# Performance work log

Measured on AMD Instinct MI355X. Metric: run time of the kernel, lower is better.

Reference implementation:

```python
import jax, jax.numpy as jnp
import numpy as np

N = 100000   # nodes
E = 640000   # edges
G = 256      # graphs in batch
H = 128      # hidden_dim
OUT = 128    # output_dim
IN = 1       # input_dim ('standard' encoding)


def _linear_init(k, din, dout):
    # torch nn.Linear default: U(-1/sqrt(din), 1/sqrt(din)) for weight and bias
    s = 1.0 / np.sqrt(din)
    kw, kb = jax.random.split(k)
    W = jax.random.uniform(kw, (din, dout), jnp.float32, -s, s)
    b = jax.random.uniform(kb, (dout,), jnp.float32, -s, s)
    return W, b


def setup_inputs() -> dict:
    key = jax.random.key(0)
    ks = jax.random.split(key, 10)
    x = jax.random.normal(ks[0], (N, IN), jnp.float32)
    edge_index = jax.random.randint(ks[1], (2, E), 0, N, dtype=jnp.int64)
    batch = jnp.sort(jax.random.randint(ks[2], (N,), 0, G, dtype=jnp.int64))
    inp = {"x": x, "edge_index": edge_index, "batch": batch}
    dims_in = [IN, H, H]  # layer 0 takes input_dim, rest take hidden_dim
    i = 3
    for l, din in enumerate(dims_in):
        inp[f"W1_{l}"], inp[f"b1_{l}"] = _linear_init(ks[i], din, H); i += 1
        inp[f"W2_{l}"], inp[f"b2_{l}"] = _linear_init(ks[i], H, H); i += 1
    inp["Wfc"], inp["bfc"] = _linear_init(ks[i], H, OUT)
    return inp


def reference(x, edge_index, batch,
              W1_0, b1_0, W2_0, b2_0,
              W1_1, b1_1, W2_1, b2_1,
              W1_2, b1_2, W2_2, b2_2,
              Wfc, bfc):
    src, dst = edge_index[0], edge_index[1]

    def gin_conv(h, W1, b1, W2, b2):
        # GINConv, eps=0: out = MLP(h + sum_{j->i} h_j)
        agg = jax.ops.segment_sum(h[src], dst, num_segments=N)  # scatter-add messages
        z = h + agg
        return jnp.maximum(z @ W1 + b1, 0.0) @ W2 + b2

    h = gin_conv(x, W1_0, b1_0, W2_0, b2_0)
    h = gin_conv(h, W1_1, b1_1, W2_1, b2_1)
    h = gin_conv(h, W1_2, b1_2, W2_2, b2_2)
    pooled = jax.ops.segment_sum(h, batch, num_segments=G)  # global_add_pool -> [G, H]
    return pooled @ Wfc + bfc  # [G, OUT]
```

## Files before the change

### kernel.cpp

```cpp
#include <hip/hip_runtime.h>

#define HH 128
#define GG 256
#define CAP 32
#define PSPLIT 16

using f32x4  = __attribute__((ext_vector_type(4))) float;
using bf16x4 = __attribute__((ext_vector_type(4))) __bf16;
using bf16x8 = __attribute__((ext_vector_type(8))) __bf16;

static __device__ __forceinline__ float bf2f(unsigned int u) {
    unsigned int x = u << 16;
    return __builtin_bit_cast(float, x);
}
static __device__ __forceinline__ unsigned short f2bf(float f) {
    __bf16 b = (__bf16)f;
    return __builtin_bit_cast(unsigned short, b);
}

__global__ __launch_bounds__(256) void prep_k(
    int* __restrict__ cnt, float* __restrict__ pooled, int n,
    const float* __restrict__ Wa, const float* __restrict__ Wb,
    const float* __restrict__ Wc, const float* __restrict__ Wd,
    const float* __restrict__ We, __bf16* __restrict__ Wp,
    const int* __restrict__ batch, int* __restrict__ bound, int zb)
{
    const int t = threadIdx.x, b = blockIdx.x;
    if (b < zb) {
        const int i = b * 256 + t;
        if (i < n) cnt[i] = 0;
        if (i < GG * HH) pooled[i] = 0.f;
    } else if (b < zb + 40) {
        const int which = b - zb;
        const int mat = which >> 3;
        const float* W = (mat == 0) ? Wa : (mat == 1) ? Wb : (mat == 2) ? Wc
                       : (mat == 3) ? Wd : We;
        const int slot = (which & 7) * 256 + t;
        const int frag = slot >> 6, lane = slot & 63;
        const int mb = frag >> 2, kb = frag & 3;
        const int col = mb * 16 + (lane & 15);
        const int k0  = kb * 32 + (lane >> 4) * 8;
        bf16x8 v;
        #pragma unroll
        for (int j = 0; j < 8; ++j) v[j] = (__bf16)W[(k0 + j) * HH + col];
        *(bf16x8*)&Wp[(size_t)mat * 16384 + slot * 8] = v;
    } else {
        const int g = t;
        int lo = 0, hi = n;
        while (lo < hi) { int m = (lo + hi) >> 1; if (batch[m] < g) lo = m + 1; else hi = m; }
        bound[g] = lo;
        if (g == 0) bound[GG] = n;
    }
}

__global__ __launch_bounds__(256) void fill_k(const int* __restrict__ src,
                                              const int* __restrict__ dst,
                                              int* __restrict__ cnt,
                                              int* __restrict__ slotbuf, int ne)
{
    int e = blockIdx.x * 256 + threadIdx.x;
    if (e < ne) {
        const int d = dst[e];
        const int off = atomicAdd(&cnt[d], 1);
        if (off < CAP) slotbuf[d * CAP + off] = src[e];
    }
}

__global__ __launch_bounds__(256) void l0_k(
    const float* __restrict__ x,
    const int* __restrict__ cnt, const int* __restrict__ slotbuf,
    const float* __restrict__ W1, const float* __restrict__ b1,
    const __bf16* __restrict__ Wp2, const float* __restrict__ b2,
    unsigned short* __restrict__ hout, int n)
{
    __shared__ __bf16 Wl[16384];
    __shared__ unsigned short tt[4][4096];
    __shared__ float b1l[HH], b2l[HH], w1l[HH];

    const int t    = threadIdx.x;
    const int lane = t & 63, wv = t >> 6;
    const int l16  = lane & 15, lq = lane >> 4;
    const int r0    = blockIdx.x * 128 + wv * 32;
    const int nodeA = r0 + l16, nodeB = r0 + 16 + l16;
    const int rowA  = min(nodeA, n - 1), rowB = min(nodeB, n - 1);
    const int swz   = (l16 & 7) << 4;

    #pragma unroll
    for (int i = 0; i < 8; ++i)
        *(int4*)&Wl[(i * 256 + t) * 8] = *(const int4*)&Wp2[(i * 256 + t) * 8];
    if (t < HH) { b2l[t] = b2[t]; b1l[t] = b1[t]; w1l[t] = W1[t]; }

    float sA, sB;
    {
        float s0 = x[rowA], s1 = 0.f, s2 = 0.f, s3 = 0.f;
        const int dA = min(cnt[rowA], CAP);
        const int* sp = &slotbuf[rowA * CAP];
        for (int j = 0; j < dA; j += 4) {
            const int i1 = min(j + 1, dA - 1), i2 = min(j + 2, dA - 1), i3 = min(j + 3, dA - 1);
            const float v0 = x[sp[j]],  v1 = x[sp[i1]];
            const float v2 = x[sp[i2]], v3 = x[sp[i3]];
            s0 += v0;
            s1 += (j + 1 < dA) ? v1 : 0.f;
            s2 += (j + 2 < dA) ? v2 : 0.f;
            s3 += (j + 3 < dA) ? v3 : 0.f;
        }
        sA = (s0 + s1) + (s2 + s3);
        s0 = x[rowB]; s1 = s2 = s3 = 0.f;
        const int dB = min(cnt[rowB], CAP);
        const int* sq = &slotbuf[rowB * CAP];
        for (int j = 0; j < dB; j += 4) {
            const int i1 = min(j + 1, dB - 1), i2 = min(j + 2, dB - 1), i3 = min(j + 3, dB - 1);
            const float v0 = x[sq[j]],  v1 = x[sq[i1]];
            const float v2 = x[sq[i2]], v3 = x[sq[i3]];
            s0 += v0;
            s1 += (j + 1 < dB) ? v1 : 0.f;
            s2 += (j + 2 < dB) ? v2 : 0.f;
            s3 += (j + 3 < dB) ? v3 : 0.f;
        }
        sB = (s0 + s1) + (s2 + s3);
    }
    __syncthreads();

    char* tl = (char*)tt[wv];
    #pragma unroll
    for (int mt = 0; mt < 8; ++mt) {
        const f32x4 w  = *(const f32x4*)&w1l[mt * 16 + lq * 4];
        const f32x4 bb = *(const f32x4*)&b1l[mt * 16 + lq * 4];
        bf16x4 pa, pb;
        #pragma unroll
        for (int r = 0; r < 4; ++r) {
            pa[r] = (__bf16)fmaxf(fmaf(sA, w[r], bb[r]), 0.f);
            pb[r] = (__bf16)fmaxf(fmaf(sB, w[r], bb[r]), 0.f);
        }
        *(bf16x4*)(tl + ((l16 * 256 + mt * 32 + lq * 8) ^ swz)) = pa;
        *(bf16x4*)(tl + (((16 + l16) * 256 + mt * 32 + lq * 8) ^ swz)) = pb;
    }
    __syncthreads();

    bf16x8 tfA[4], tfB[4];
    #pragma unroll
    for (int kb = 0; kb < 4; ++kb) {
        tfA[kb] = *(const bf16x8*)(tl + ((l16 * 256 + kb * 64 + lq * 16) ^ swz));
        tfB[kb] = *(const bf16x8*)(tl + (((16 + l16) * 256 + kb * 64 + lq * 16) ^ swz));
    }
    f32x4 a2A[8], a2B[8];
    #pragma unroll
    for (int mb = 0; mb < 8; ++mb) {
        const f32x4 bb = *(const f32x4*)&b2l[mb * 16 + lq * 4];
        a2A[mb] = bb; a2B[mb] = bb;
    }
    #pragma unroll
    for (int mb = 0; mb < 8; ++mb)
        #pragma unroll
        for (int kb = 0; kb < 4; ++kb) {
            const bf16x8 wf = *(const bf16x8*)&Wl[((mb * 4 + kb) * 64 + lane) * 8];
            a2A[mb] = __builtin_amdgcn_mfma_f32_16x16x32_bf16(wf, tfA[kb], a2A[mb], 0, 0, 0);
            a2B[mb] = __builtin_amdgcn_mfma_f32_16x16x32_bf16(wf, tfB[kb], a2B[mb], 0, 0, 0);
        }
    if (nodeA < n) {
        #pragma unroll
        for (int mb = 0; mb < 8; ++mb) {
            bf16x4 p;
            #pragma unroll
            for (int r = 0; r < 4; ++r) p[r] = (__bf16)a2A[mb][r];
            *(bf16x4*)&hout[(size_t)nodeA * HH + mb * 16 + lq * 4] = p;
        }
    }
    if (nodeB < n) {
        #pragma unroll
        for (int mb = 0; mb < 8; ++mb) {
            bf16x4 p;
            #pragma unroll
            for (int r = 0; r < 4; ++r) p[r] = (__bf16)a2B[mb][r];
            *(bf16x4*)&hout[(size_t)nodeB * HH + mb * 16 + lq * 4] = p;
        }
    }
}

static __device__ __forceinline__ void agg_body(
    const unsigned short* __restrict__ h, const int* __restrict__ cnt,
    const int* __restrict__ slotbuf, unsigned short* __restrict__ z, int n)
{
    const int wave = (blockIdx.x * 256 + threadIdx.x) >> 6;
    const int lane = threadIdx.x & 63;
    const int half = lane >> 5, sl = lane & 31;
    const int nw   = (gridDim.x * 256) >> 6;
    const int npairs = (n + 1) >> 1;
    const uint2* h8 = (const uint2*)h;
    uint2* z8 = (uint2*)z;

    for (int pr = wave; pr < npairs; pr += nw) {
        const int node = min(2 * pr + half, n - 1);
        const int deg = min(cnt[node], CAP);
        const int* sp = &slotbuf[node * CAP];
        const uint2 su = h8[(size_t)node * 32 + sl];
        float a0 = bf2f(su.x & 0xffff), a1 = bf2f(su.x >> 16);
        float a2 = bf2f(su.y & 0xffff), a3 = bf2f(su.y >> 16);
        float b0 = 0.f, b1 = 0.f, b2 = 0.f, b3 = 0.f;
        float c0 = 0.f, c1 = 0.f, c2 = 0.f, c3 = 0.f;
        float d0 = 0.f, d1 = 0.f, d2 = 0.f, d3 = 0.f;
        for (int j = 0; j < deg; j += 4) {
            const int i1 = min(j + 1, deg - 1), i2 = min(j + 2, deg - 1), i3 = min(j + 3, deg - 1);
            const uint2 v0 = h8[(size_t)sp[j]  * 32 + sl];
            const uint2 v1 = h8[(size_t)sp[i1] * 32 + sl];
            const uint2 v2 = h8[(size_t)sp[i2] * 32 + sl];
            const uint2 v3 = h8[(size_t)sp[i3] * 32 + sl];
            a0 += bf2f(v0.x & 0xffff); a1 += bf2f(v0.x >> 16);
            a2 += bf2f(v0.y & 0xffff); a3 += bf2f(v0.y >> 16);
            const bool m1 = (j + 1 < deg), m2 = (j + 2 < deg), m3 = (j + 3 < deg);
            b0 += m1 ? bf2f(v1.x & 0xffff) : 0.f; b1 += m1 ? bf2f(v1.x >> 16) : 0.f;
            b2 += m1 ? bf2f(v1.y & 0xffff) : 0.f; b3 += m1 ? bf2f(v1.y >> 16) : 0.f;
            c0 += m2 ? bf2f(v2.x & 0xffff) : 0.f; c1 += m2 ? bf2f(v2.x >> 16) : 0.f;
            c2 += m2 ? bf2f(v2.y & 0xffff) : 0.f; c3 += m2 ? bf2f(v2.y >> 16) : 0.f;
            d0 += m3 ? bf2f(v3.x & 0xffff) : 0.f; d1 += m3 ? bf2f(v3.x >> 16) : 0.f;
            d2 += m3 ? bf2f(v3.y & 0xffff) : 0.f; d3 += m3 ? bf2f(v3.y >> 16) : 0.f;
        }
        const float s0 = (a0 + b0) + (c0 + d0);
        const float s1 = (a1 + b1) + (c1 + d1);
        const float s2 = (a2 + b2) + (c2 + d2);
        const float s3 = (a3 + b3) + (c3 + d3);
        uint2 o;
        o.x = (unsigned int)f2bf(s0) | ((unsigned int)f2bf(s1) << 16);
        o.y = (unsigned int)f2bf(s2) | ((unsigned int)f2bf(s3) << 16);
        z8[(size_t)node * 32 + sl] = o;
    }
}
__global__ __launch_bounds__(256) void agg1_k(const unsigned short* h, const int* cnt,
                                              const int* slotbuf, unsigned short* z, int n)
{ agg_body(h, cnt, slotbuf, z, n); }
__global__ __launch_bounds__(256) void agg2_k(const unsigned short* h, const int* cnt,
                                              const int* slotbuf, unsigned short* z, int n)
{ agg_body(h, cnt, slotbuf, z, n); }

static __device__ __forceinline__ void mlp_body4(
    const unsigned short* __restrict__ z,
    const __bf16* __restrict__ Wp1, const float* __restrict__ b1,
    const __bf16* __restrict__ Wp2, const float* __restrict__ b2,
    unsigned short* __restrict__ hout, int n)
{
    __shared__ unsigned short tt[4][4096];

    const int t    = threadIdx.x;
    const int lane = t & 63, wv = t >> 6;
    const int l16  = lane & 15, lq = lane >> 4;
    const int r0    = blockIdx.x * 128 + wv * 32;
    const int nodeA = r0 + l16, nodeB = r0 + 16 + l16;
    const int rowA  = min(nodeA, n - 1), rowB = min(nodeB, n - 1);
    const int swz   = (l16 & 7) << 4;

    bf16x8 zfA[4], zfB[4];
    #pragma unroll
    for (int kb = 0; kb < 4; ++kb) {
        zfA[kb] = *(const bf16x8*)&z[(size_t)rowA * HH + kb * 32 + lq * 8];
        zfB[kb] = *(const bf16x8*)&z[(size_t)rowB * HH + kb * 32 + lq * 8];
    }

    char* tl = (char*)tt[wv];

    #pragma unroll
    for (int mt = 0; mt < 8; ++mt) {
        const f32x4 bb = *(const f32x4*)&b1[mt * 16 + lq * 4];
        f32x4 aA = bb, aB = bb;
        #pragma unroll
        for (int kb = 0; kb < 4; ++kb) {
            const bf16x8 wf = *(const bf16x8*)&Wp1[((mt * 4 + kb) * 64 + lane) * 8];
            aA = __builtin_amdgcn_mfma_f32_16x16x32_bf16(wf, zfA[kb], aA, 0, 0, 0);
            aB = __builtin_amdgcn_mfma_f32_16x16x32_bf16(wf, zfB[kb], aB, 0, 0, 0);
        }
        bf16x4 pa, pb;
        #pragma unroll
        for (int r = 0; r < 4; ++r) {
            pa[r] = (__bf16)fmaxf(aA[r], 0.f);
            pb[r] = (__bf16)fmaxf(aB[r], 0.f);
        }
        *(bf16x4*)(tl + ((l16 * 256 + mt * 32 + lq * 8) ^ swz)) = pa;
        *(bf16x4*)(tl + (((16 + l16) * 256 + mt * 32 + lq * 8) ^ swz)) = pb;
    }

    bf16x8 tfA[4], tfB[4];
    #pragma unroll
    for (int kb = 0; kb < 4; ++kb) {
        tfA[kb] = *(const bf16x8*)(tl + ((l16 * 256 + kb * 64 + lq * 16) ^ swz));
        tfB[kb] = *(const bf16x8*)(tl + (((16 + l16) * 256 + kb * 64 + lq * 16) ^ swz));
    }
    #pragma unroll
    for (int mb = 0; mb < 8; ++mb) {
        const f32x4 bb = *(const f32x4*)&b2[mb * 16 + lq * 4];
        f32x4 aA = bb, aB = bb;
        #pragma unroll
        for (int kb = 0; kb < 4; ++kb) {
            const bf16x8 wf = *(const bf16x8*)&Wp2[((mb * 4 + kb) * 64 + lane) * 8];
            aA = __builtin_amdgcn_mfma_f32_16x16x32_bf16(wf, tfA[kb], aA, 0, 0, 0);
            aB = __builtin_amdgcn_mfma_f32_16x16x32_bf16(wf, tfB[kb], aB, 0, 0, 0);
        }
        if (nodeA < n) {
            bf16x4 p;
            #pragma unroll
            for (int r = 0; r < 4; ++r) p[r] = (__bf16)aA[r];
            *(bf16x4*)&hout[(size_t)nodeA * HH + mb * 16 + lq * 4] = p;
        }
        if (nodeB < n) {
            bf16x4 p;
            #pragma unroll
            for (int r = 0; r < 4; ++r) p[r] = (__bf16)aB[r];
            *(bf16x4*)&hout[(size_t)nodeB * HH + mb * 16 + lq * 4] = p;
        }
    }
}

__global__ __launch_bounds__(256, 4) void mlp1_k(const unsigned short* z,
                                                 const __bf16* Wp1, const float* b1,
                                                 const __bf16* Wp2, const float* b2,
                                                 unsigned short* h, int n)
{ mlp_body4(z, Wp1, b1, Wp2, b2, h, n); }

__global__ __launch_bounds__(256, 4) void mlp2_k(const unsigned short* z,
                                                 const __bf16* Wp1, const float* b1,
                                                 const __bf16* Wp2, const float* b2,
                                                 unsigned short* h, int n)
{ mlp_body4(z, Wp1, b1, Wp2, b2, h, n); }

__global__ __launch_bounds__(64) void pool_k(const unsigned short* __restrict__ h,
                                             const int* __restrict__ bound,
                                             float* __restrict__ pooled)
{
    const int g = blockIdx.x >> 4;
    const int s = blockIdx.x & (PSPLIT - 1);
    const int t = threadIdx.x;
    const int half = t >> 5, sl = t & 31;
    const int rb = bound[g], re = bound[g + 1];
    const int len = re - rb;
    const int i0 = rb + (int)(((long)len * s) / PSPLIT);
    const int i1 = rb + (int)(((long)len * (s + 1)) / PSPLIT);
    const uint2* h8 = (const uint2*)h;

    float p0 = 0.f, p1 = 0.f, p2 = 0.f, p3 = 0.f;
    float q0 = 0.f, q1 = 0.f, q2 = 0.f, q3 = 0.f;
    int r = i0 + half;
    for (; r + 2 < i1; r += 4) {
        const uint2 a = h8[(size_t)r * 32 + sl];
        const uint2 b = h8[(size_t)(r + 2) * 32 + sl];
        p0 += bf2f(a.x & 0xffff); p1 += bf2f(a.x >> 16);
        p2 += bf2f(a.y & 0xffff); p3 += bf2f(a.y >> 16);
        q0 += bf2f(b.x & 0xffff); q1 += bf2f(b.x >> 16);
        q2 += bf2f(b.y & 0xffff); q3 += bf2f(b.y >> 16);
    }
    if (r < i1) {
        const uint2 a = h8[(size_t)r * 32 + sl];
        p0 += bf2f(a.x & 0xffff); p1 += bf2f(a.x >> 16);
        p2 += bf2f(a.y & 0xffff); p3 += bf2f(a.y >> 16);
    }
    p0 += q0; p1 += q1; p2 += q2; p3 += q3;
    if (i0 + half < i1) {
        float* p = &pooled[g * HH + sl * 4];
        unsafeAtomicAdd(p + 0, p0);
        unsafeAtomicAdd(p + 1, p1);
        unsafeAtomicAdd(p + 2, p2);
        unsafeAtomicAdd(p + 3, p3);
    }
}

__global__ __launch_bounds__(128) void fc_k(const float* __restrict__ pooled,
                                            const float* __restrict__ Wfc,
                                            const float* __restrict__ bfc,
                                            float* __restrict__ out)
{
    __shared__ float p[HH];
    const int g = blockIdx.x, k = threadIdx.x;
    p[k] = pooled[g * HH + k];
    __syncthreads();
    float acc = bfc[k];
    #pragma unroll 8
    for (int j = 0; j < HH; ++j) acc = fmaf(p[j], Wfc[j * HH + k], acc);
    out[g * HH + k] = acc;
}

extern "C" void kernel_launch(void* const* d_in, const int* in_sizes, int n_in,
                              void* d_out, int out_size, void* d_ws, size_t ws_size,
                              hipStream_t stream)
{
    const float* x     = (const float*)d_in[0];
    const int*   ei    = (const int*)d_in[1];
    const int*   batch = (const int*)d_in[2];
    const float* W1_0 = (const float*)d_in[3];
    const float* b1_0 = (const float*)d_in[4];
    const float* W2_0 = (const float*)d_in[5];
    const float* b2_0 = (const float*)d_in[6];
    const float* W1_1 = (const float*)d_in[7];
    const float* b1_1 = (const float*)d_in[8];
    const float* W2_1 = (const float*)d_in[9];
    const float* b2_1 = (const float*)d_in[10];
    const float* W1_2 = (const float*)d_in[11];
    const float* b1_2 = (const float*)d_in[12];
    const float* W2_2 = (const float*)d_in[13];
    const float* b2_2 = (const float*)d_in[14];
    const float* Wfc  = (const float*)d_in[15];
    const float* bfc  = (const float*)d_in[16];

    const int N = in_sizes[0];
    const int E = in_sizes[1] / 2;
    const int* src = ei;
    const int* dst = ei + E;

    char* p = (char*)d_ws;
    #define CARVE(ty, name, count) ty* name = (ty*)p; p += (((size_t)(count) * sizeof(ty)) + 255) & ~(size_t)255;
    CARVE(unsigned short, hA,     (size_t)N * HH)
    CARVE(unsigned short, hB,     (size_t)N * HH)
    CARVE(float,          pooled, GG * HH)
    CARVE(int,            cnt,    N)
    CARVE(int,            slotbuf,(size_t)N * CAP)
    CARVE(int,            bound,  GG + 1)
    CARVE(__bf16,         Wp,     5 * 16384)
    #undef CARVE
    float* outp = (float*)d_out;

    const int gblk = (N + 127) / 128;
    const int zb   = (N + 255) / 256;

    prep_k<<<zb + 41, 256, 0, stream>>>(cnt, pooled, N, W2_0, W1_1, W2_1, W1_2, W2_2,
                                        Wp, batch, bound, zb);
    fill_k<<<(E + 255) / 256, 256, 0, stream>>>(src, dst, cnt, slotbuf, E);

    l0_k<<<gblk, 256, 0, stream>>>(x, cnt, slotbuf, W1_0, b1_0, Wp, b2_0, hA, N);

    agg1_k<<<2048, 256, 0, stream>>>(hA, cnt, slotbuf, hB, N);
    mlp1_k<<<gblk, 256, 0, stream>>>(hB, Wp + 16384, b1_1, Wp + 2 * 16384, b2_1, hA, N);

    agg2_k<<<2048, 256, 0, stream>>>(hA, cnt, slotbuf, hB, N);
    mlp2_k<<<gblk, 256, 0, stream>>>(hB, Wp + 3 * 16384, b1_2, Wp + 4 * 16384, b2_2, hA, N);

    pool_k<<<GG * PSPLIT, 64, 0, stream>>>(hA, bound, pooled);
    fc_k<<<GG, HH, 0, stream>>>(pooled, Wfc, bfc, outp);
}
```

Measured before the change: 211.7 us.

## Make MLP kernels persistent with LDS-resident weights and prefetched node tiles

Turns the two hidden-layer MLP kernels into persistent 512-thread blocks, a grid of at most 256, that load both weight matrices and biases into shared memory once. Each block then loops over 256-node tiles and prefetches the next tile's aggregated features into registers while it computes the current one. This removes repeated global/L2 weight fetches per MFMA and hides the z-load latency. In exchange, LDS use rises to about 129 KB per block, which limits occupancy to one block per CU, and register pressure grows from the prefetch buffers. It also drops a redundant barrier in the layer-0 kernel, where each wave only reads its own scratch tile.

New measurement: 280.9 us. 1.33x slower.

```diff
diff --git a/kernel.cpp b/kernel.cpp
--- a/kernel.cpp
+++ b/kernel.cpp
@@ -135,7 +135,6 @@
         *(bf16x4*)(tl + ((l16 * 256 + mt * 32 + lq * 8) ^ swz)) = pa;
         *(bf16x4*)(tl + (((16 + l16) * 256 + mt * 32 + lq * 8) ^ swz)) = pb;
     }
-    __syncthreads();
 
     bf16x8 tfA[4], tfB[4];
     #pragma unroll
@@ -232,93 +231,132 @@
                                               const int* slotbuf, unsigned short* z, int n)
 { agg_body(h, cnt, slotbuf, z, n); }
 
-static __device__ __forceinline__ void mlp_body4(
+static __device__ __forceinline__ void loadz(
+    const unsigned short* __restrict__ z, int rowA, int rowB, int lq,
+    bf16x8* zfA, bf16x8* zfB)
+{
+    #pragma unroll
+    for (int kb = 0; kb < 4; ++kb) {
+        zfA[kb] = *(const bf16x8*)&z[(size_t)rowA * HH + kb * 32 + lq * 8];
+        zfB[kb] = *(const bf16x8*)&z[(size_t)rowB * HH + kb * 32 + lq * 8];
+    }
+}
+
+static __device__ __forceinline__ void mlp_pipe(
     const unsigned short* __restrict__ z,
     const __bf16* __restrict__ Wp1, const float* __restrict__ b1,
     const __bf16* __restrict__ Wp2, const float* __restrict__ b2,
     unsigned short* __restrict__ hout, int n)
 {
-    __shared__ unsigned short tt[4][4096];
+    __shared__ __bf16 Wl1[16384], Wl2[16384];
+    __shared__ unsigned short tt[8][4096];
+    __shared__ float b1l[HH], b2l[HH];
 
     const int t    = threadIdx.x;
     const int lane = t & 63, wv = t >> 6;
     const int l16  = lane & 15, lq = lane >> 4;
-    const int r0    = blockIdx.x * 128 + wv * 32;
-    const int nodeA = r0 + l16, nodeB = r0 + 16 + l16;
-    const int rowA  = min(nodeA, n - 1), rowB = min(nodeB, n - 1);
-    const int swz   = (l16 & 7) << 4;
+    const int swz  = (l16 & 7) << 4;
+    const int ntiles = (n + 255) >> 8;
+
+    #pragma unroll
+    for (int i = 0; i < 4; ++i) {
+        *(int4*)&Wl1[(i * 512 + t) * 8] = *(const int4*)&Wp1[(i * 512 + t) * 8];
+        *(int4*)&Wl2[(i * 512 + t) * 8] = *(const int4*)&Wp2[(i * 512 + t) * 8];
+    }
+    if (t < HH) b1l[t] = b1[t];
+    else if (t < 2 * HH) b2l[t - HH] = b2[t - HH];
+
+    char* tl = (char*)tt[wv];
+
+    int tile = blockIdx.x;
+    if (tile >= ntiles) return;
 
     bf16x8 zfA[4], zfB[4];
-    #pragma unroll
-    for (int kb = 0; kb < 4; ++kb) {
-        zfA[kb] = *(const bf16x8*)&z[(size_t)rowA * HH + kb * 32 + lq * 8];
-        zfB[kb] = *(const bf16x8*)&z[(size_t)rowB * HH + kb * 32 + lq * 8];
-    }
-
-    char* tl = (char*)tt[wv];
-
-    #pragma unroll
-    for (int mt = 0; mt < 8; ++mt) {
-        const f32x4 bb = *(const f32x4*)&b1[mt * 16 + lq * 4];
-        f32x4 aA = bb, aB = bb;
+    {
+        const int r0 = tile * 256 + wv * 32;
+        loadz(z, min(r0 + l16, n - 1), min(r0 + 16 + l16, n - 1), lq, zfA, zfB);
+    }
+    __syncthreads();
+
+    while (true) {
+        const int r0 = tile * 256 + wv * 32;
+        const int nodeA = r0 + l16, nodeB = r0 + 16 + l16;
+
+        #pragma unroll
+        for (int mt = 0; mt < 8; ++mt) {
+            const f32x4 bb = *(const f32x4*)&b1l[mt * 16 + lq * 4];
+            f32x4 aA = bb, aB = bb;
+            #pragma unroll
+            for (int kb = 0; kb < 4; ++kb) {
+                const bf16x8 wf = *(const bf16x8*)&Wl1[((mt * 4 + kb) * 64 + lane) * 8];
+                aA = __builtin_amdgcn_mfma_f32_16x16x32_bf16(wf, zfA[kb], aA, 0, 0, 0);
+                aB = __builtin_amdgcn_mfma_f32_16x16x32_bf16(wf, zfB[kb], aB, 0, 0, 0);
+            }
+            bf16x4 pa, pb;
+            #pragma unroll
+            for (int r = 0; r < 4; ++r) {
+                pa[r] = (__bf16)fmaxf(aA[r], 0.f);
+                pb[r] = (__bf16)fmaxf(aB[r], 0.f);
+            }
+            *(bf16x4*)(tl + ((l16 * 256 + mt * 32 + lq * 8) ^ swz)) = pa;
+            *(bf16x4*)(tl + (((16 + l16) * 256 + mt * 32 + lq * 8) ^ swz)) = pb;
+        }
+
+        const int next = tile + gridDim.x;
+        bf16x8 nzA[4], nzB[4];
+        if (next < ntiles) {
+            const int nr0 = next * 256 + wv * 32;
+            loadz(z, min(nr0 + l16, n - 1), min(nr0 + 16 + l16, n - 1), lq, nzA, nzB);
+        }
+
+        bf16x8 tfA[4], tfB[4];
         #pragma unroll
         for (int kb = 0; kb < 4; ++kb) {
-            const bf16x8 wf = *(const bf16x8*)&Wp1[((mt * 4 + kb) * 64 + lane) * 8];
-            aA = __builtin_amdgcn_mfma_f32_16x16x32_bf16(wf, zfA[kb], aA, 0, 0, 0);
-            aB = __builtin_amdgcn_mfma_f32_16x16x32_bf16(wf, zfB[kb], aB, 0, 0, 0);
-        }
-        bf16x4 pa, pb;
-        #pragma unroll
-        for (int r = 0; r < 4; ++r) {
-            pa[r] = (__bf16)fmaxf(aA[r], 0.f);
-            pb[r] = (__bf16)fmaxf(aB[r], 0.f);
-        }
-        *(bf16x4*)(tl + ((l16 * 256 + mt * 32 + lq * 8) ^ swz)) = pa;
-        *(bf16x4*)(tl + (((16 + l16) * 256 + mt * 32 + lq * 8) ^ swz)) = pb;
-    }
-
-    bf16x8 tfA[4], tfB[4];
-    #pragma unroll
-    for (int kb = 0; kb < 4; ++kb) {
-        tfA[kb] = *(const bf16x8*)(tl + ((l16 * 256 + kb * 64 + lq * 16) ^ swz));
-        tfB[kb] = *(const bf16x8*)(tl + (((16 + l16) * 256 + kb * 64 + lq * 16) ^ swz));
-    }
-    #pragma unroll
-    for (int mb = 0; mb < 8; ++mb) {
-        const f32x4 bb = *(const f32x4*)&b2[mb * 16 + lq * 4];
-        f32x4 aA = bb, aB = bb;
-        #pragma unroll
-        for (int kb = 0; kb < 4; ++kb) {
-            const bf16x8 wf = *(const bf16x8*)&Wp2[((mb * 4 + kb) * 64 + lane) * 8];
-            aA = __builtin_amdgcn_mfma_f32_16x16x32_bf16(wf, tfA[kb], aA, 0, 0, 0);
-            aB = __builtin_amdgcn_mfma_f32_16x16x32_bf16(wf, tfB[kb], aB, 0, 0, 0);
-        }
-        if (nodeA < n) {
-            bf16x4 p;
+            tfA[kb] = *(const bf16x8*)(tl + ((l16 * 256 + kb * 64 + lq * 16) ^ swz));
+            tfB[kb] = *(const bf16x8*)(tl + (((16 + l16) * 256 + kb * 64 + lq * 16) ^ swz));
+        }
+        #pragma unroll
+        for (int mb = 0; mb < 8; ++mb) {
+            const f32x4 bb = *(const f32x4*)&b2l[mb * 16 + lq * 4];
+            f32x4 aA = bb, aB = bb;
             #pragma unroll
-            for (int r = 0; r < 4; ++r) p[r] = (__bf16)aA[r];
-            *(bf16x4*)&hout[(size_t)nodeA * HH + mb * 16 + lq * 4] = p;
-        }
-        if (nodeB < n) {
-            bf16x4 p;
-            #pragma unroll
-            for (int r = 0; r < 4; ++r) p[r] = (__bf16)aB[r];
-            *(bf16x4*)&hout[(size_t)nodeB * HH + mb * 16 + lq * 4] = p;
-        }
-    }
-}
-
-__global__ __launch_bounds__(256, 4) void mlp1_k(const unsigned short* z,
-                                                 const __bf16* Wp1, const float* b1,
-                                                 const __bf16* Wp2, const float* b2,
-                                                 unsigned short* h, int n)
-{ mlp_body4(z, Wp1, b1, Wp2, b2, h, n); }
-
-__global__ __launch_bounds__(256, 4) void mlp2_k(const unsigned short* z,
-                                                 const __bf16* Wp1, const float* b1,
-                                                 const __bf16* Wp2, const float* b2,
-                                                 unsigned short* h, int n)
-{ mlp_body4(z, Wp1, b1, Wp2, b2, h, n); }
+            for (int kb = 0; kb < 4; ++kb) {
+                const bf16x8 wf = *(const bf16x8*)&Wl2[((mb * 4 + kb) * 64 + lane) * 8];
+                aA = __builtin_amdgcn_mfma_f32_16x16x32_bf16(wf, tfA[kb], aA, 0, 0, 0);
+                aB = __builtin_amdgcn_mfma_f32_16x16x32_bf16(wf, tfB[kb], aB, 0, 0, 0);
+            }
+            if (nodeA < n) {
+                bf16x4 p;
+                #pragma unroll
+                for (int r = 0; r < 4; ++r) p[r] = (__bf16)aA[r];
+                *(bf16x4*)&hout[(size_t)nodeA * HH + mb * 16 + lq * 4] = p;
+            }
+            if (nodeB < n) {
+                bf16x4 p;
+                #pragma unroll
+                for (int r = 0; r < 4; ++r) p[r] = (__bf16)aB[r];
+                *(bf16x4*)&hout[(size_t)nodeB * HH + mb * 16 + lq * 4] = p;
+            }
+        }
+
+        if (next >= ntiles) break;
+        tile = next;
+        #pragma unroll
+        for (int kb = 0; kb < 4; ++kb) { zfA[kb] = nzA[kb]; zfB[kb] = nzB[kb]; }
+    }
+}
+
+__global__ __launch_bounds__(512) void mlp1_k(const unsigned short* z,
+                                              const __bf16* Wp1, const float* b1,
+                                              const __bf16* Wp2, const float* b2,
+                                              unsigned short* h, int n)
+{ mlp_pipe(z, Wp1, b1, Wp2, b2, h, n); }
+
+__global__ __launch_bounds__(512) void mlp2_k(const unsigned short* z,
+                                              const __bf16* Wp1, const float* b1,
+                                              const __bf16* Wp2, const float* b2,
+                                              unsigned short* h, int n)
+{ mlp_pipe(z, Wp1, b1, Wp2, b2, h, n); }
 
 __global__ __launch_bounds__(64) void pool_k(const unsigned short* __restrict__ h,
                                              const int* __restrict__ bound,
@@ -416,6 +454,8 @@
 
     const int gblk = (N + 127) / 128;
     const int zb   = (N + 255) / 256;
+    const int ntiles = (N + 255) / 256;
+    const int mgrid = min(256, ntiles);
 
     prep_k<<<zb + 41, 256, 0, stream>>>(cnt, pooled, N, W2_0, W1_1, W2_1, W1_2, W2_2,
                                         Wp, batch, bound, zb);
@@ -424,10 +464,10 @@
     l0_k<<<gblk, 256, 0, stream>>>(x, cnt, slotbuf, W1_0, b1_0, Wp, b2_0, hA, N);
 
     agg1_k<<<2048, 256, 0, stream>>>(hA, cnt, slotbuf, hB, N);
-    mlp1_k<<<gblk, 256, 0, stream>>>(hB, Wp + 16384, b1_1, Wp + 2 * 16384, b2_1, hA, N);
+    mlp1_k<<<mgrid, 512, 0, stream>>>(hB, Wp + 16384, b1_1, Wp + 2 * 16384, b2_1, hA, N);
 
     agg2_k<<<2048, 256, 0, stream>>>(hA, cnt, slotbuf, hB, N);
-    mlp2_k<<<gblk, 256, 0, stream>>>(hB, Wp + 3 * 16384, b1_2, Wp + 4 * 16384, b2_2, hA, N);
+    mlp2_k<<<mgrid, 512, 0, stream>>>(hB, Wp + 3 * 16384, b1_2, Wp + 4 * 16384, b2_2, hA, N);
 
     pool_k<<<GG * PSPLIT, 64, 0, stream>>>(hA, bound, pooled);
     fc_k<<<GG, HH, 0, stream>>>(pooled, Wfc, bfc, outp);
```
